# Performance work log

Hardware: AMD Instinct MI355X
Metric: run time of the kernel (lower is better)

The kernel has to match this reference:

```python
import jax, jax.numpy as jnp
import numpy as np

V, E, H, T, B = 32000, 1024, 1024, 128, 128


def setup_inputs() -> dict:
    key = jax.random.key(0)
    ks = jax.random.split(key, 12)
    inp = {
        "batch_a": jax.random.randint(ks[0], (T, B), 0, V),
        "batch_b": jax.random.randint(ks[1], (T, B), 0, V),
        "h0_a": jax.random.normal(ks[2], (B, H), jnp.float32),
        "c0_a": jax.random.normal(ks[3], (B, H), jnp.float32),
        "h0_b": jax.random.normal(ks[4], (B, H), jnp.float32),
        "c0_b": jax.random.normal(ks[5], (B, H), jnp.float32),
    }
    # shared encoder parameters (encoder_a and encoder_b are the same weights)
    emb = jax.random.normal(ks[6], (V, E), jnp.float32) * 0.02
    emb = emb.at[0].set(0.0)  # padding_idx=0
    scale = 1.0 / np.sqrt(H)
    inp["emb"] = emb
    inp["w_ih"] = jax.random.uniform(ks[7], (4 * H, E), jnp.float32, -scale, scale)
    inp["w_hh"] = jax.random.uniform(ks[8], (4 * H, H), jnp.float32, -scale, scale)
    b_ih = jax.random.uniform(ks[9], (4 * H,), jnp.float32, -scale, scale)
    b_hh = jax.random.uniform(ks[10], (4 * H,), jnp.float32, -scale, scale)
    # forget-gate bias filled with 2.5 (initialize_parameters fills [H:2H])
    inp["b_ih"] = b_ih.at[H:2 * H].set(2.5)
    inp["b_hh"] = b_hh.at[H:2 * H].set(2.5)
    return inp


def _lstm_final_hidden(ids, h0, c0, emb, w_ih, w_hh, b):
    # ids: [T, B]; returns final hidden state [B, H]
    x_seq = emb[ids]  # [T, B, E]

    def step(carry, x):
        h, c = carry
        gates = x @ w_ih.T + h @ w_hh.T + b  # [B, 4H]
        i, f, g, o = jnp.split(gates, 4, axis=-1)  # PyTorch gate order i,f,g,o
        c_new = jax.nn.sigmoid(f) * c + jax.nn.sigmoid(i) * jnp.tanh(g)
        h_new = jax.nn.sigmoid(o) * jnp.tanh(c_new)
        return (h_new, c_new), None

    (h_fin, _), _ = jax.lax.scan(step, (h0, c0), x_seq)
    return h_fin


def reference(batch_a, batch_b, h0_a, c0_a, h0_b, c0_b, emb, w_ih, w_hh, b_ih, b_hh):
    b = b_ih + b_hh
    enc_a = _lstm_final_hidden(batch_a, h0_a, c0_a, emb, w_ih, w_hh, b)
    enc_b = _lstm_final_hidden(batch_b, h0_b, c0_b, emb, w_ih, w_hh, b)
    # similarity: exp(-L1 distance per batch row)
    prediction = jnp.exp(-jnp.sum(jnp.abs(enc_a - enc_b), axis=1))  # [B]
    return prediction
```

## Files before the change

### kernel.cpp

```cpp
#include <hip/hip_runtime.h>


typedef unsigned char u8;
typedef unsigned short u16;
typedef unsigned long long u64;
typedef __attribute__((ext_vector_type(2))) unsigned long long u64x2;
typedef __attribute__((ext_vector_type(4))) float f32x4;

__device__ __forceinline__ u8 f2e4m3(float f) {
  unsigned ui = __builtin_bit_cast(unsigned, f);
  unsigned s = (ui >> 24) & 0x80u;
  float a = fabsf(f);
  if (a >= 448.f) return (u8)(s | 0x7Eu);
  if (a < 0.015625f) {
    int m = (int)rintf(a * 512.f);
    return (u8)(s | (unsigned)m);
  }
  unsigned au = ui & 0x7fffffffu;
  int e = (int)(au >> 23) - 127;
  float mm = __builtin_bit_cast(float, (au & 0x007fffffu) | 0x3f800000u);
  int q = (int)rintf((mm - 1.0f) * 8.0f);
  unsigned body = (unsigned)(((e + 7) << 3) + q);
  if (body > 0x7Eu) body = 0x7Eu;
  return (u8)(s | body);
}
__device__ __forceinline__ float e4m32f(u8 b) {
  unsigned e = (b >> 3) & 15u;
  unsigned m = b & 7u;
  float mag = (e == 0) ? (float)m * 0.001953125f
                       : __builtin_bit_cast(float, (e + 117u) << 23) * (float)(8u + m);
  return (b & 0x80u) ? -mag : mag;
}

__global__ __launch_bounds__(256) void prep_wf_kernel(const float* __restrict__ w_ih,
                                                      const float* __restrict__ w_hh,
                                                      u8* __restrict__ Wf) {
  unsigned idx = blockIdx.x * 256u + threadIdx.x;
  unsigned l = idx & 63u;
  unsigned kcg = (idx >> 6) & 63u;
  unsigned f = (idx >> 12) & 3u;
  unsigned nh = idx >> 14;
  unsigned r = f * 1024u + nh * 16u + (l & 15u);
  unsigned k0 = kcg * 32u + ((l >> 4) << 3);
  const float* src = (k0 < 1024u) ? (w_ih + (size_t)r * 1024u + k0)
                                  : (w_hh + (size_t)r * 1024u + (k0 - 1024u));
  float4 v0 = *(const float4*)src;
  float4 v1 = *(const float4*)(src + 4);
  u64 o = 0;
  o |= (u64)f2e4m3(v0.x * 16.f);
  o |= (u64)f2e4m3(v0.y * 16.f) << 8;
  o |= (u64)f2e4m3(v0.z * 16.f) << 16;
  o |= (u64)f2e4m3(v0.w * 16.f) << 24;
  o |= (u64)f2e4m3(v1.x * 16.f) << 32;
  o |= (u64)f2e4m3(v1.y * 16.f) << 40;
  o |= (u64)f2e4m3(v1.z * 16.f) << 48;
  o |= (u64)f2e4m3(v1.w * 16.f) << 56;
  *(u64*)(Wf + (size_t)idx * 8u) = o;
}

__global__ __launch_bounds__(256) void prep_state_kernel(
    const float* __restrict__ h0a, const float* __restrict__ h0b,
    const float* __restrict__ c0a, const float* __restrict__ c0b,
    const float* __restrict__ b_ih, const float* __restrict__ b_hh,
    const int* __restrict__ batch_a, const int* __restrict__ batch_b,
    const float* __restrict__ emb,
    float* __restrict__ bias, u8* __restrict__ hb0, float* __restrict__ cb,
    u8* __restrict__ xb0) {
  unsigned i = blockIdx.x * 256u + threadIdx.x;
  unsigned r = i >> 10;
  unsigned k = i & 1023u;
  float hv = (r < 128u) ? h0a[i] : h0b[i - 131072u];
  float cv = (r < 128u) ? c0a[i] : c0b[i - 131072u];
  hb0[i] = f2e4m3(hv);
  cb[i] = cv;
  int token = (r < 128u) ? batch_a[r] : batch_b[r - 128u];
  xb0[i] = f2e4m3(emb[(size_t)token * 1024u + k] * 16.f);
  if (i < 4096u) bias[i] = b_ih[i] + b_hh[i];
}

__global__ __launch_bounds__(256) void lstm_step_kernel(
    const int* __restrict__ batch_a, const int* __restrict__ batch_b,
    const float* __restrict__ emb, const u8* __restrict__ Wf,
    const float* __restrict__ bias,
    const u8* __restrict__ x_in, u8* __restrict__ x_next,
    const u8* __restrict__ h_in, u8* __restrict__ h_out,
    float* __restrict__ cbuf, int t) {
  __shared__ u8 As[2][2][64][128];
  __shared__ float Gs[2][64][68];

  const int tid = threadIdx.x;
  const int lane = tid & 63;
  const int w = tid >> 6;
  const int kg = w >> 1, wn = w & 1;
  const int m = blockIdx.x >> 6;
  const int nh = blockIdx.x & 63;

  f32x4 g0 = {0.f, 0.f, 0.f, 0.f};
  const bool do_g = (t + 1 < 128);
  if (do_g) {
    int r = blockIdx.x;
    int token = (r < 128) ? batch_a[(t + 1) * 128 + r]
                          : batch_b[(t + 1) * 128 + (r - 128)];
    g0 = __builtin_nontemporal_load(
        (const f32x4*)(emb + (size_t)token * 1024 + tid * 4));
  }

  const int skg = tid >> 7;
  const int gtid = tid & 127;
  const int srow = gtid >> 1;
  const int qb = (gtid & 1) << 6;
  const int wswz = (srow & 15) << 3;
  char* dstA0 = (char*)&As[skg][0][0][0] + srow * 128;
  char* dstA1 = (char*)&As[skg][1][0][0] + srow * 128;
  const u8* aBase = (skg == 0 ? x_in : h_in)
                    + ((size_t)(m * 64 + srow) << 10) + qb;

  const u8* wf0 = Wf + ((((size_t)(nh * 4 + wn * 2) * 64) + kg * 32) << 9) + lane * 8;
  const u8* wf1 = wf0 + (64 << 9);

  const int fr = lane & 15;
  const int fkb = (lane >> 4) << 3;
  const int rswz = fr << 3;
  const char* A0 = (const char*)&As[kg][0][0][0];
  const char* A1 = (const char*)&As[kg][1][0][0];

  f32x4 acc[4][2];
#pragma unroll
  for (int a_ = 0; a_ < 4; ++a_)
#pragma unroll
    for (int b_ = 0; b_ < 2; ++b_) acc[a_][b_] = (f32x4){0.f, 0.f, 0.f, 0.f};

  u64x2 av[4];
  u64 brc[8], brn[8];
#pragma unroll
  for (int q = 0; q < 4; ++q) av[q] = *(const u64x2*)(aBase + q * 16);
#pragma unroll
  for (int kcl = 0; kcl < 4; ++kcl) {
    brc[kcl * 2]     = *(const u64*)(wf0 + (kcl << 9));
    brc[kcl * 2 + 1] = *(const u64*)(wf1 + (kcl << 9));
  }

#pragma unroll
  for (int it = 0; it < 8; ++it) {
    {
      char* dst = (it & 1) ? dstA1 : dstA0;
#pragma unroll
      for (int q = 0; q < 4; ++q) {
        *(u64*)(dst + ((qb + q * 16)     ^ wswz)) = av[q][0];
        *(u64*)(dst + ((qb + q * 16 + 8) ^ wswz)) = av[q][1];
      }
    }
    __syncthreads();
    if (it < 7) {
      const u8* an = aBase + (it + 1) * 128;
#pragma unroll
      for (int q = 0; q < 4; ++q) av[q] = *(const u64x2*)(an + q * 16);
#pragma unroll
      for (int kcl = 0; kcl < 4; ++kcl) {
        brn[kcl * 2]     = *(const u64*)(wf0 + (((it + 1) * 4 + kcl) << 9));
        brn[kcl * 2 + 1] = *(const u64*)(wf1 + (((it + 1) * 4 + kcl) << 9));
      }
    }
    const char* ab = (it & 1) ? A1 : A0;
#pragma unroll
    for (int kcl = 0; kcl < 4; ++kcl) {
      long b0 = __builtin_bit_cast(long, brc[kcl * 2]);
      long b1 = __builtin_bit_cast(long, brc[kcl * 2 + 1]);
#pragma unroll
      for (int frg = 0; frg < 4; ++frg) {
        u64 afu = *(const u64*)(ab + (frg * 16 + fr) * 128 + ((kcl * 32 + fkb) ^ rswz));
        long a0 = __builtin_bit_cast(long, afu);
        acc[frg][0] = __builtin_amdgcn_mfma_f32_16x16x32_fp8_fp8(a0, b0, acc[frg][0], 0, 0, 0);
        acc[frg][1] = __builtin_amdgcn_mfma_f32_16x16x32_fp8_fp8(a0, b1, acc[frg][1], 0, 0, 0);
      }
    }
    if (it < 7) {
#pragma unroll
      for (int p = 0; p < 8; ++p) brc[p] = brn[p];
    }
  }

  {
    const int hi4 = (lane >> 4) << 2;
#pragma unroll
    for (int frg = 0; frg < 4; ++frg)
#pragma unroll
      for (int fc = 0; fc < 2; ++fc)
#pragma unroll
        for (int r_ = 0; r_ < 4; ++r_)
          Gs[kg][frg * 16 + hi4 + r_][(wn * 2 + fc) * 16 + fr] = acc[frg][fc][r_];
  }
  __syncthreads();

  {
    const int crow = tid >> 2;
    const int u0 = (tid & 3) << 2;
    const int R2 = m * 64 + crow;
    const int gj = nh * 16 + u0;
    size_t ci = (size_t)R2 * 1024 + gj;
    f32x4 c_old = *(const f32x4*)(cbuf + ci);
    f32x4 bi = *(const f32x4*)(bias + gj);
    f32x4 bf = *(const f32x4*)(bias + 1024 + gj);
    f32x4 bg = *(const f32x4*)(bias + 2048 + gj);
    f32x4 bo = *(const f32x4*)(bias + 3072 + gj);
    f32x4 cnv;
    unsigned pk = 0;
#pragma unroll
    for (int uu = 0; uu < 4; ++uu) {
      int cix = u0 + uu;
      float iv = Gs[0][crow][cix]      * 0.00390625f + Gs[1][crow][cix]      * 0.0625f + bi[uu];
      float fv = Gs[0][crow][16 + cix] * 0.00390625f + Gs[1][crow][16 + cix] * 0.0625f + bf[uu];
      float gv = Gs[0][crow][32 + cix] * 0.00390625f + Gs[1][crow][32 + cix] * 0.0625f + bg[uu];
      float ov = Gs[0][crow][48 + cix] * 0.00390625f + Gs[1][crow][48 + cix] * 0.0625f + bo[uu];
      float si = 1.f / (1.f + __expf(-iv));
      float sf = 1.f / (1.f + __expf(-fv));
      float so = 1.f / (1.f + __expf(-ov));
      float cn = sf * c_old[uu] + si * tanhf(gv);
      cnv[uu] = cn;
      float hn = so * tanhf(cn);
      pk |= ((unsigned)f2e4m3(hn)) << (uu * 8);
    }
    *(f32x4*)(cbuf + ci) = cnv;
    *(unsigned*)(h_out + ci) = pk;
  }

  if (do_g) {
    int r = blockIdx.x;
    unsigned o = 0;
    o |= (unsigned)f2e4m3(g0[0] * 16.f);
    o |= (unsigned)f2e4m3(g0[1] * 16.f) << 8;
    o |= (unsigned)f2e4m3(g0[2] * 16.f) << 16;
    o |= (unsigned)f2e4m3(g0[3] * 16.f) << 24;
    *(unsigned*)(x_next + (size_t)r * 1024 + tid * 4) = o;
  }
}

__global__ __launch_bounds__(256) void finalize_kernel(const u8* __restrict__ h,
                                                       float* __restrict__ out) {
  int b = blockIdx.x;
  int tid = threadIdx.x;
  const u8* ha = h + (size_t)b * 1024;
  const u8* hb = h + (size_t)(b + 128) * 1024;
  float s = 0.f;
  for (int j = tid; j < 1024; j += 256) s += fabsf(e4m32f(ha[j]) - e4m32f(hb[j]));
  __shared__ float red[256];
  red[tid] = s;
  __syncthreads();
  for (int off = 128; off > 0; off >>= 1) {
    if (tid < off) red[tid] += red[tid + off];
    __syncthreads();
  }
  if (tid == 0) out[b] = expf(-red[0]);
}

extern "C" void kernel_launch(void* const* d_in, const int* in_sizes, int n_in,
                              void* d_out, int out_size, void* d_ws, size_t ws_size,
                              hipStream_t stream) {
  const int* batch_a = (const int*)d_in[0];
  const int* batch_b = (const int*)d_in[1];
  const float* h0_a = (const float*)d_in[2];
  const float* c0_a = (const float*)d_in[3];
  const float* h0_b = (const float*)d_in[4];
  const float* c0_b = (const float*)d_in[5];
  const float* emb  = (const float*)d_in[6];
  const float* w_ih = (const float*)d_in[7];
  const float* w_hh = (const float*)d_in[8];
  const float* b_ih = (const float*)d_in[9];
  const float* b_hh = (const float*)d_in[10];

  char* ws = (char*)d_ws;
  u8*    Wf   = (u8*)(ws);
  float* bias = (float*)(ws + 8388608);
  u8*    xb0  = (u8*)(ws + 8404992);
  u8*    xb1  = (u8*)(ws + 8667136);
  u8*    hb0  = (u8*)(ws + 8929280);
  u8*    hb1  = (u8*)(ws + 9191424);
  float* cb   = (float*)(ws + 9453568);

  prep_wf_kernel<<<4096, 256, 0, stream>>>(w_ih, w_hh, Wf);
  prep_state_kernel<<<1024, 256, 0, stream>>>(h0_a, h0_b, c0_a, c0_b, b_ih, b_hh,
                                              batch_a, batch_b, emb, bias, hb0, cb, xb0);
  u8* xb[2] = {xb0, xb1};
  u8* hb[2] = {hb0, hb1};
  for (int t = 0; t < 128; ++t) {
    lstm_step_kernel<<<256, 256, 0, stream>>>(batch_a, batch_b, emb, Wf, bias,
                                              xb[t & 1], xb[(t + 1) & 1],
                                              hb[t & 1], hb[(t + 1) & 1], cb, t);
  }
  finalize_kernel<<<128, 256, 0, stream>>>(hb[0], (float*)d_out);
}
```

Baseline: 1.415 ms.

## Halve per-block row tile to launch 512 blocks per LSTM step

Each step kernel now handles 32 batch rows instead of 64, doubling the grid to 512 blocks so more of the GPU's compute units are busy for the small per-step GEMM. Shared-memory tiles, accumulators, the cell-update mapping (2 units per thread) and the next-step embedding prefetch (split into halves across block pairs) are all resized to match. The cost is that the fp8 weight tiles are read by twice as many blocks, doubling weight traffic per step, and there is less MFMA work per weight load.

```diff
diff --git a/kernel.cpp b/kernel.cpp
--- a/kernel.cpp
+++ b/kernel.cpp
@@ -5,6 +5,7 @@
 typedef unsigned short u16;
 typedef unsigned long long u64;
 typedef __attribute__((ext_vector_type(2))) unsigned long long u64x2;
+typedef __attribute__((ext_vector_type(2))) float f32x2;
 typedef __attribute__((ext_vector_type(4))) float f32x4;
 
 __device__ __forceinline__ u8 f2e4m3(float f) {
@@ -85,8 +86,8 @@
     const u8* __restrict__ x_in, u8* __restrict__ x_next,
     const u8* __restrict__ h_in, u8* __restrict__ h_out,
     float* __restrict__ cbuf, int t) {
-  __shared__ u8 As[2][2][64][128];
-  __shared__ float Gs[2][64][68];
+  __shared__ u8 As[2][2][32][128];
+  __shared__ float Gs[2][32][68];
 
   const int tid = threadIdx.x;
   const int lane = tid & 63;
@@ -96,24 +97,25 @@
   const int nh = blockIdx.x & 63;
 
   f32x4 g0 = {0.f, 0.f, 0.f, 0.f};
-  const bool do_g = (t + 1 < 128);
+  const bool do_g = (t + 1 < 128) && (tid < 128);
   if (do_g) {
-    int r = blockIdx.x;
+    int r = blockIdx.x >> 1;
+    int half = blockIdx.x & 1;
     int token = (r < 128) ? batch_a[(t + 1) * 128 + r]
                           : batch_b[(t + 1) * 128 + (r - 128)];
     g0 = __builtin_nontemporal_load(
-        (const f32x4*)(emb + (size_t)token * 1024 + tid * 4));
+        (const f32x4*)(emb + (size_t)token * 1024 + half * 512 + tid * 4));
   }
 
   const int skg = tid >> 7;
   const int gtid = tid & 127;
-  const int srow = gtid >> 1;
-  const int qb = (gtid & 1) << 6;
+  const int srow = gtid >> 2;
+  const int q32 = (gtid & 3) << 5;
   const int wswz = (srow & 15) << 3;
   char* dstA0 = (char*)&As[skg][0][0][0] + srow * 128;
   char* dstA1 = (char*)&As[skg][1][0][0] + srow * 128;
   const u8* aBase = (skg == 0 ? x_in : h_in)
-                    + ((size_t)(m * 64 + srow) << 10) + qb;
+                    + ((size_t)(m * 32 + srow) << 10) + q32;
 
   const u8* wf0 = Wf + ((((size_t)(nh * 4 + wn * 2) * 64) + kg * 32) << 9) + lane * 8;
   const u8* wf1 = wf0 + (64 << 9);
@@ -124,16 +126,16 @@
   const char* A0 = (const char*)&As[kg][0][0][0];
   const char* A1 = (const char*)&As[kg][1][0][0];
 
-  f32x4 acc[4][2];
-#pragma unroll
-  for (int a_ = 0; a_ < 4; ++a_)
+  f32x4 acc[2][2];
+#pragma unroll
+  for (int a_ = 0; a_ < 2; ++a_)
 #pragma unroll
     for (int b_ = 0; b_ < 2; ++b_) acc[a_][b_] = (f32x4){0.f, 0.f, 0.f, 0.f};
 
-  u64x2 av[4];
+  u64x2 av[2];
   u64 brc[8], brn[8];
-#pragma unroll
-  for (int q = 0; q < 4; ++q) av[q] = *(const u64x2*)(aBase + q * 16);
+  av[0] = *(const u64x2*)(aBase);
+  av[1] = *(const u64x2*)(aBase + 16);
 #pragma unroll
   for (int kcl = 0; kcl < 4; ++kcl) {
     brc[kcl * 2]     = *(const u64*)(wf0 + (kcl << 9));
@@ -144,17 +146,16 @@
   for (int it = 0; it < 8; ++it) {
     {
       char* dst = (it & 1) ? dstA1 : dstA0;
-#pragma unroll
-      for (int q = 0; q < 4; ++q) {
-        *(u64*)(dst + ((qb + q * 16)     ^ wswz)) = av[q][0];
-        *(u64*)(dst + ((qb + q * 16 + 8) ^ wswz)) = av[q][1];
-      }
+      *(u64*)(dst + ((q32 + 0)  ^ wswz)) = av[0][0];
+      *(u64*)(dst + ((q32 + 8)  ^ wswz)) = av[0][1];
+      *(u64*)(dst + ((q32 + 16) ^ wswz)) = av[1][0];
+      *(u64*)(dst + ((q32 + 24) ^ wswz)) = av[1][1];
     }
     __syncthreads();
     if (it < 7) {
       const u8* an = aBase + (it + 1) * 128;
-#pragma unroll
-      for (int q = 0; q < 4; ++q) av[q] = *(const u64x2*)(an + q * 16);
+      av[0] = *(const u64x2*)(an);
+      av[1] = *(const u64x2*)(an + 16);
 #pragma unroll
       for (int kcl = 0; kcl < 4; ++kcl) {
         brn[kcl * 2]     = *(const u64*)(wf0 + (((it + 1) * 4 + kcl) << 9));
@@ -167,7 +168,7 @@
       long b0 = __builtin_bit_cast(long, brc[kcl * 2]);
       long b1 = __builtin_bit_cast(long, brc[kcl * 2 + 1]);
 #pragma unroll
-      for (int frg = 0; frg < 4; ++frg) {
+      for (int frg = 0; frg < 2; ++frg) {
         u64 afu = *(const u64*)(ab + (frg * 16 + fr) * 128 + ((kcl * 32 + fkb) ^ rswz));
         long a0 = __builtin_bit_cast(long, afu);
         acc[frg][0] = __builtin_amdgcn_mfma_f32_16x16x32_fp8_fp8(a0, b0, acc[frg][0], 0, 0, 0);
@@ -183,7 +184,7 @@
   {
     const int hi4 = (lane >> 4) << 2;
 #pragma unroll
-    for (int frg = 0; frg < 4; ++frg)
+    for (int frg = 0; frg < 2; ++frg)
 #pragma unroll
       for (int fc = 0; fc < 2; ++fc)
 #pragma unroll
@@ -193,45 +194,43 @@
   __syncthreads();
 
   {
-    const int crow = tid >> 2;
-    const int u0 = (tid & 3) << 2;
-    const int R2 = m * 64 + crow;
+    const int crow = tid >> 3;
+    const int u0 = (tid & 7) << 1;
+    const int R2 = m * 32 + crow;
     const int gj = nh * 16 + u0;
     size_t ci = (size_t)R2 * 1024 + gj;
-    f32x4 c_old = *(const f32x4*)(cbuf + ci);
-    f32x4 bi = *(const f32x4*)(bias + gj);
-    f32x4 bf = *(const f32x4*)(bias + 1024 + gj);
-    f32x4 bg = *(const f32x4*)(bias + 2048 + gj);
-    f32x4 bo = *(const f32x4*)(bias + 3072 + gj);
-    f32x4 cnv;
-    unsigned pk = 0;
-#pragma unroll
-    for (int uu = 0; uu < 4; ++uu) {
+    f32x2 c_old = *(const f32x2*)(cbuf + ci);
+    f32x2 cnv;
+    u16 pk = 0;
+#pragma unroll
+    for (int uu = 0; uu < 2; ++uu) {
       int cix = u0 + uu;
-      float iv = Gs[0][crow][cix]      * 0.00390625f + Gs[1][crow][cix]      * 0.0625f + bi[uu];
-      float fv = Gs[0][crow][16 + cix] * 0.00390625f + Gs[1][crow][16 + cix] * 0.0625f + bf[uu];
-      float gv = Gs[0][crow][32 + cix] * 0.00390625f + Gs[1][crow][32 + cix] * 0.0625f + bg[uu];
-      float ov = Gs[0][crow][48 + cix] * 0.00390625f + Gs[1][crow][48 + cix] * 0.0625f + bo[uu];
+      int gjc = gj + uu;
+      float iv = Gs[0][crow][cix]      * 0.00390625f + Gs[1][crow][cix]      * 0.0625f + bias[gjc];
+      float fv = Gs[0][crow][16 + cix] * 0.00390625f + Gs[1][crow][16 + cix] * 0.0625f + bias[1024 + gjc];
+      float gv = Gs[0][crow][32 + cix] * 0.00390625f + Gs[1][crow][32 + cix] * 0.0625f + bias[2048 + gjc];
+      float ov = Gs[0][crow][48 + cix] * 0.00390625f + Gs[1][crow][48 + cix] * 0.0625f + bias[3072 + gjc];
       float si = 1.f / (1.f + __expf(-iv));
       float sf = 1.f / (1.f + __expf(-fv));
       float so = 1.f / (1.f + __expf(-ov));
       float cn = sf * c_old[uu] + si * tanhf(gv);
       cnv[uu] = cn;
       float hn = so * tanhf(cn);
-      pk |= ((unsigned)f2e4m3(hn)) << (uu * 8);
-    }
-    *(f32x4*)(cbuf + ci) = cnv;
-    *(unsigned*)(h_out + ci) = pk;
+      pk |= ((u16)f2e4m3(hn)) << (uu * 8);
+    }
+    *(f32x2*)(cbuf + ci) = cnv;
+    *(u16*)(h_out + ci) = pk;
   }
 
   if (do_g) {
-    int r = blockIdx.x;
+    int r = blockIdx.x >> 1;
+    int half = blockIdx.x & 1;
     unsigned o = 0;
     o |= (unsigned)f2e4m3(g0[0] * 16.f);
     o |= (unsigned)f2e4m3(g0[1] * 16.f) << 8;
     o |= (unsigned)f2e4m3(g0[2] * 16.f) << 16;
     o |= (unsigned)f2e4m3(g0[3] * 16.f) << 24;
-    *(unsigned*)(x_next + (size_t)r * 1024 + tid * 4) = o;
+    *(unsigned*)(x_next + (size_t)r * 1024 + half * 512 + tid * 4) = o;
   }
 }
 
@@ -283,7 +282,7 @@
   u8* xb[2] = {xb0, xb1};
   u8* hb[2] = {hb0, hb1};
   for (int t = 0; t < 128; ++t) {
-    lstm_step_kernel<<<256, 256, 0, stream>>>(batch_a, batch_b, emb, Wf, bias,
+    lstm_step_kernel<<<512, 256, 0, stream>>>(batch_a, batch_b, emb, Wf, bias,
                                               xb[t & 1], xb[(t + 1) & 1],
                                               hb[t & 1], hb[(t + 1) & 1], cb, t);
   }
```

Result: faster. 1.303 ms (-7.9%).
